# Kernel optimization log

Measured on AMD Instinct MI355X. Metric: run time of the kernel, lower is better.

The kernel has to match this reference:

```python
import jax, jax.numpy as jnp
import numpy as np

H = 4096          # hidden_size
I = 11008         # intermediate_size
G = 128           # AWQ group_size
# AWQ interleaved nibble order within each packed int32
_ORDER = jnp.array([0, 4, 1, 5, 2, 6, 3, 7], dtype=jnp.int32) * 4


def _mk_lin(key, K, N):
    k1, k2, k3 = jax.random.split(key, 3)
    qw = jax.random.randint(k1, (K, N // 8), 0, 100, dtype=jnp.int32)
    qz = jax.random.randint(k2, (K // G, N // 8), 0, 100, dtype=jnp.int32)
    sc = jax.random.normal(k3, (K // G, N), dtype=jnp.float32) * 0.02
    return qw, qz, sc


def setup_inputs() -> dict:
    key = jax.random.key(0)
    ks = jax.random.split(key, 7)
    x = jax.random.normal(ks[0], (8, 16, H), dtype=jnp.float32)
    ln1_w = jnp.ones((H,), dtype=jnp.float32)
    ln2_w = jnp.ones((H,), dtype=jnp.float32)
    qkv_qw, qkv_qz, qkv_sc = _mk_lin(ks[1], H, 3 * H)
    o_qw, o_qz, o_sc = _mk_lin(ks[2], H, H)
    gu_qw, gu_qz, gu_sc = _mk_lin(ks[3], H, 2 * I)
    dn_qw, dn_qz, dn_sc = _mk_lin(ks[4], I, H)
    return dict(x=x, ln1_w=ln1_w, ln2_w=ln2_w,
                qkv_qw=qkv_qw, qkv_qz=qkv_qz, qkv_sc=qkv_sc,
                o_qw=o_qw, o_qz=o_qz, o_sc=o_sc,
                gu_qw=gu_qw, gu_qz=gu_qz, gu_sc=gu_sc,
                dn_qw=dn_qw, dn_qz=dn_qz, dn_sc=dn_sc)


def rmsnorm(x, w, eps=1e-6):
    return x * jax.lax.rsqrt(jnp.mean(x * x, axis=-1, keepdims=True) + eps) * w


def dequant(qw, qz, sc):
    # qw: [K, N//8] int32 -> [K, N]; qz: [K//G, N//8] -> [K//G, N]
    K = qw.shape[0]
    N = sc.shape[1]
    w = ((qw[:, :, None] >> _ORDER) & 0xF).reshape(K, N).astype(sc.dtype)
    z = ((qz[:, :, None] >> _ORDER) & 0xF).reshape(K // G, N).astype(sc.dtype)
    return (w - jnp.repeat(z, G, axis=0)) * jnp.repeat(sc, G, axis=0)


def lite_linear(x, qw, qz, sc):
    return x @ dequant(qw, qz, sc)


def reference(x, ln1_w, ln2_w,
              qkv_qw, qkv_qz, qkv_sc,
              o_qw, o_qz, o_sc,
              gu_qw, gu_qz, gu_sc,
              dn_qw, dn_qz, dn_sc):
    residual = x
    h = rmsnorm(x, ln1_w)
    h = lite_linear(h, qkv_qw, qkv_qz, qkv_sc)[..., :H]  # mock attn: take q slice
    h = lite_linear(h, o_qw, o_qz, o_sc)
    h = residual + h
    residual = h
    h = rmsnorm(h, ln2_w)
    gate_up = lite_linear(h, gu_qw, gu_qz, gu_sc)
    gate, up = gate_up[..., :I], gate_up[..., I:]
    h = lite_linear(jax.nn.silu(gate) * up, dn_qw, dn_qz, dn_sc)
    return residual + h
```

## Files before the change

### kernel.cpp

```cpp
#include <hip/hip_runtime.h>

typedef unsigned int   u32;
typedef unsigned short u16;

typedef _Float16 h2  __attribute__((ext_vector_type(2)));
typedef _Float16 h8  __attribute__((ext_vector_type(8)));
typedef float    f32x4 __attribute__((ext_vector_type(4)));

#define M_TOK 128

__device__ __forceinline__ u16 f2h_(float f) {
    _Float16 h = (_Float16)f; return __builtin_bit_cast(u16, h);
}
__device__ __forceinline__ float h2f_(u16 b) {
    _Float16 h = __builtin_bit_cast(_Float16, b); return (float)h;
}
__device__ __forceinline__ void acc8(uint4 v, float* s) {
#pragma unroll
    for (int i = 0; i < 4; ++i) {
        u32 w = ((const u32*)&v)[i];
        s[2 * i]     += h2f_((u16)(w & 0xFFFF));
        s[2 * i + 1] += h2f_((u16)(w >> 16));
    }
}

__constant__ int SHC[8] = {0, 16, 4, 20, 8, 24, 12, 28};

__launch_bounds__(256)
__global__ void pack_zs(const int* __restrict__ qz, const float* __restrict__ sc,
                        u32* __restrict__ zs, int qws, int scs, int Ncols, int total) {
    const int idx = blockIdx.x * 256 + threadIdx.x;
    if (idx >= total) return;
    const int g = idx / Ncols, n = idx - g * Ncols;
    const u32 d = (u32)qz[(size_t)g * qws + (n >> 3)];
    const u32 zj = (d >> SHC[n & 7]) & 15u;
    const u32 mz = 0xE400u | zj;
    const u16 sh = f2h_(sc[(size_t)g * scs + n]);
    zs[(size_t)g * Ncols + n] = mz | ((u32)sh << 16);
}


__launch_bounds__(256)
__global__ void rmsnorm_k(const float* __restrict__ in, const float* __restrict__ w,
                          u16* __restrict__ out) {
    const int row = blockIdx.x;
    const float* x = in + (size_t)row * 4096;
    float ss = 0.f;
#pragma unroll
    for (int j = 0; j < 16; ++j) {
        float v = x[threadIdx.x + 256 * j];
        ss += v * v;
    }
#pragma unroll
    for (int off = 32; off > 0; off >>= 1) ss += __shfl_down(ss, off, 64);
    __shared__ float ws4[4];
    if ((threadIdx.x & 63) == 0) ws4[threadIdx.x >> 6] = ss;
    __syncthreads();
    float total = ws4[0] + ws4[1] + ws4[2] + ws4[3];
    float r = rsqrtf(total * (1.f / 4096.f) + 1e-6f);
    const int mt = row >> 4, l16 = row & 15;
#pragma unroll
    for (int c2 = 0; c2 < 2; ++c2) {
        int c = threadIdx.x * 2 + c2;
        int kb = c >> 2, qq = c & 3;
        u16 o8[8];
#pragma unroll
        for (int j = 0; j < 8; ++j) {
            int i = c * 8 + j;
            o8[j] = f2h_(x[i] * r * w[i]);
        }
        *(uint4*)(out + ((size_t)(kb * 8 + mt) * 64 + qq * 16 + l16) * 8) = *(const uint4*)o8;
    }
}

__launch_bounds__(256, 4)
__global__ void gemm_awq(const u16* __restrict__ A, const u32* __restrict__ zs,
                         const int* __restrict__ qw, u16* __restrict__ part,
                         int qws, int N, int K, int kchunk) {
    __shared__ __align__(16) char ldsB[4 * 4608];

    const int tid = threadIdx.x, w = tid >> 6, lane = tid & 63;
    const int q = lane >> 4, l16 = lane & 15;
    const int mh = w >> 1;
    const int bx = (blockIdx.x & 7) * (gridDim.x >> 3) + (blockIdx.x >> 3);
    const int n0w = bx * 64 + (w & 1) * 32;
    const int pc0 = n0w >> 3;
    const int kp = lane & 31, h = lane >> 5;
    const int sk = blockIdx.y, kc0 = sk * kchunk, kend = min(kc0 + kchunk, K);

    char* myB   = ldsB + w * 4608;
    char* wbase = myB + kp * 4;
    const u16* Ala = A + lane * 8;
    const int* qws_base = qw + pc0;
    const u32* zsA = zs + n0w + h * 8;
    const u32* zsB = zs + n0w + 16 + h * 8;

    f32x4 acc[4][2] = {};
    uint4 za0, za1, zb0, zb1;

    auto ldraw = [&](int k0) -> uint4 {
        return *(const uint4*)(qws_base + (size_t)(k0 + lane) * qws);
    };
    auto loadzs = [&](int g) {
        za0 = *(const uint4*)(zsA + (size_t)g * N);
        za1 = *(const uint4*)(zsA + (size_t)g * N + 4);
        zb0 = *(const uint4*)(zsB + (size_t)g * N);
        zb1 = *(const uint4*)(zsB + (size_t)g * N + 4);
    };
    auto route = [&](uint4 rv, u32* d) {
        const int i0 = kp * 8, i1 = i0 + 4;
        int b00 = __builtin_amdgcn_ds_bpermute(i0, (int)rv.x);
        int b10 = __builtin_amdgcn_ds_bpermute(i0, (int)rv.y);
        int b20 = __builtin_amdgcn_ds_bpermute(i0, (int)rv.z);
        int b30 = __builtin_amdgcn_ds_bpermute(i0, (int)rv.w);
        int b01 = __builtin_amdgcn_ds_bpermute(i1, (int)rv.x);
        int b11 = __builtin_amdgcn_ds_bpermute(i1, (int)rv.y);
        int b21 = __builtin_amdgcn_ds_bpermute(i1, (int)rv.z);
        int b31 = __builtin_amdgcn_ds_bpermute(i1, (int)rv.w);
        d[0] = (u32)(h ? b10 : b00);
        d[1] = (u32)(h ? b11 : b01);
        d[2] = (u32)(h ? b30 : b20);
        d[3] = (u32)(h ? b31 : b21);
    };
    auto emit8 = [&](u32 w0, u32 w1, int nb, uint4 z0, uint4 z1) {
        char* bb = wbase + nb * 144;
        u32 w0s = w0 >> 4, w1s = w1 >> 4;
        auto em = [&](int j, u32 a0, u32 a1, int b, u32 zsj) {
            h2 mz = __builtin_bit_cast(h2, __builtin_amdgcn_perm(zsj, zsj, 0x01000100u));
            h2 s2 = __builtin_bit_cast(h2, __builtin_amdgcn_perm(zsj, zsj, 0x03020302u));
            u32 t = __builtin_amdgcn_perm(a1, a0, (u32)(b | ((b + 4) << 16)));
            u32 u = (t & 0x000F000Fu) | 0x64006400u;
            h2 v = (__builtin_bit_cast(h2, u) + mz) * s2;
            *(u32*)(bb + j * 144) = __builtin_bit_cast(u32, v);
        };
        em(0, w0, w1, 0, z0.x);  em(4, w0, w1, 1, z1.x);
        em(1, w0, w1, 2, z0.y);  em(5, w0, w1, 3, z1.y);
        em(2, w0s, w1s, 0, z0.z); em(6, w0s, w1s, 1, z1.z);
        em(3, w0s, w1s, 2, z0.w); em(7, w0s, w1s, 3, z1.w);
    };
    auto dq = [&](uint4 rv) {
        u32 qd[4];
        route(rv, qd);
        emit8(qd[0], qd[1], h * 8, za0, za1);
        emit8(qd[2], qd[3], 16 + h * 8, zb0, zb1);
    };
    auto lda = [&](int k, uint4(&dst)[2][4]) {
        const int kb = k >> 5;
#pragma unroll
        for (int c = 0; c < 2; ++c)
#pragma unroll
            for (int mt = 0; mt < 4; ++mt)
                dst[c][mt] = *(const uint4*)(Ala + (size_t)((kb + c) * 8 + mh * 4 + mt) * 512);
    };

    uint4 rv_n = {0, 0, 0, 0};

    loadzs(kc0 >> 7);
    uint4 rv0 = ldraw(kc0);
    if (kc0 + 64 < kend) rv_n = ldraw(kc0 + 64);
    {
        u32 qd[4];
        route(rv0, qd);
        emit8(qd[0], qd[1], h * 8, za0, za1);
        emit8(qd[2], qd[3], 16 + h * 8, zb0, zb1);
    }
    if (((kc0 + 64) & 127) == 0 && kc0 + 64 < kend)
        loadzs((kc0 + 64) >> 7);

    for (int k0 = kc0; k0 < kend; k0 += 64) {
        __syncthreads();
        const bool kn1 = (k0 + 64) < kend, kn2 = (k0 + 128) < kend;
        uint4 af[2][4];
        lda(k0, af);
        uint4 bv[2][2];
#pragma unroll
        for (int c = 0; c < 2; ++c)
#pragma unroll
            for (int nt = 0; nt < 2; ++nt)
                bv[c][nt] = *(const uint4*)(myB + (nt * 16 + l16) * 144 + c * 64 + q * 16);
        uint4 rv_f = {0, 0, 0, 0};
        if (kn2) rv_f = ldraw(k0 + 128);
        if (kn1) {
            u32 qd[4];
            route(rv_n, qd);
            emit8(qd[0], qd[1], h * 8, za0, za1);
            emit8(qd[2], qd[3], 16 + h * 8, zb0, zb1);
        }
        if (kn2 && (((k0 + 128) & 127) == 0))
            loadzs((k0 + 128) >> 7);
#pragma unroll
        for (int c = 0; c < 2; ++c)
#pragma unroll
            for (int mt = 0; mt < 4; ++mt)
#pragma unroll
                for (int nt = 0; nt < 2; ++nt)
                    acc[mt][nt] = __builtin_amdgcn_mfma_f32_16x16x32_f16(
                        __builtin_bit_cast(h8, af[c][mt]),
                        __builtin_bit_cast(h8, bv[c][nt]),
                        acc[mt][nt], 0, 0, 0);
        rv_n = rv_f;
    }

    u16* pp = part + (size_t)sk * M_TOK * N;
#pragma unroll
    for (int mt = 0; mt < 4; ++mt)
#pragma unroll
        for (int nt = 0; nt < 2; ++nt) {
            const int n = n0w + nt * 16 + l16;
#pragma unroll
            for (int r = 0; r < 4; ++r) {
                const int m = (mh * 4 + mt) * 16 + q * 4 + r;
                pp[(size_t)m * N + n] = f2h_(acc[mt][nt][r]);
            }
        }
}

__launch_bounds__(256)
__global__ void reduce_to_afrag(const u16* __restrict__ part, u16* __restrict__ out,
                                int SK) {
    const int idx = blockIdx.x * 256 + threadIdx.x;
    const int m = idx >> 9, c = idx & 511;
    float s[8] = {};
    for (int k = 0; k < SK; ++k)
        acc8(*(const uint4*)(part + (size_t)k * 524288 + (size_t)m * 4096 + c * 8), s);
    const int kb = c >> 2, qq = c & 3, mt = m >> 4, l16 = m & 15;
    u16 o8[8];
#pragma unroll
    for (int j = 0; j < 8; ++j) o8[j] = f2h_(s[j]);
    *(uint4*)(out + ((size_t)(kb * 8 + mt) * 64 + qq * 16 + l16) * 8) = *(const uint4*)o8;
}

__launch_bounds__(256)
__global__ void reduce_add_f32(const u16* __restrict__ part, const float* __restrict__ resin,
                               float* __restrict__ out, int SK) {
    const int idx = blockIdx.x * 256 + threadIdx.x;
    const size_t base = (size_t)idx * 8;
    float s[8];
    *(float4*)&s[0] = *(const float4*)(resin + base);
    *(float4*)&s[4] = *(const float4*)(resin + base + 4);
    for (int k = 0; k < SK; ++k)
        acc8(*(const uint4*)(part + (size_t)k * 524288 + base), s);
    *(float4*)(out + base)     = *(const float4*)&s[0];
    *(float4*)(out + base + 4) = *(const float4*)&s[4];
}

__launch_bounds__(256)
__global__ void silu_mul(const u16* __restrict__ part, u16* __restrict__ act, int SK) {
    const int idx = blockIdx.x * 256 + threadIdx.x;
    const int m = idx / 1376, c = idx - m * 1376;
    const int nb = c * 8;
    float g[8] = {}, u[8] = {};
    for (int k = 0; k < SK; ++k) {
        const size_t base = (size_t)k * 2818048 + (size_t)m * 22016 + nb;
        acc8(*(const uint4*)(part + base), g);
        acc8(*(const uint4*)(part + base + 11008), u);
    }
    const int kb = nb >> 5, qq = (nb >> 3) & 3, mt = m >> 4, l16 = m & 15;
    u16 o8[8];
#pragma unroll
    for (int j = 0; j < 8; ++j) {
        float a = g[j] / (1.f + __expf(-g[j])) * u[j];
        o8[j] = f2h_(a);
    }
    *(uint4*)(act + ((size_t)(kb * 8 + mt) * 64 + qq * 16 + l16) * 8) = *(const uint4*)o8;
}

extern "C" void kernel_launch(void* const* d_in, const int* in_sizes, int n_in,
                              void* d_out, int out_size, void* d_ws, size_t ws_size,
                              hipStream_t stream) {
    const float* x      = (const float*)d_in[0];
    const float* ln1_w  = (const float*)d_in[1];
    const float* ln2_w  = (const float*)d_in[2];
    const int*   qkv_qw = (const int*)d_in[3];
    const int*   qkv_qz = (const int*)d_in[4];
    const float* qkv_sc = (const float*)d_in[5];
    const int*   o_qw   = (const int*)d_in[6];
    const int*   o_qz   = (const int*)d_in[7];
    const float* o_sc   = (const float*)d_in[8];
    const int*   gu_qw  = (const int*)d_in[9];
    const int*   gu_qz  = (const int*)d_in[10];
    const float* gu_sc  = (const float*)d_in[11];
    const int*   dn_qw  = (const int*)d_in[12];
    const int*   dn_qz  = (const int*)d_in[13];
    const float* dn_sc  = (const float*)d_in[14];
    float* out = (float*)d_out;

    char* ws = (char*)d_ws;
    u16*   pbuf = (u16*)(ws);
    u32*   zsb  = (u32*)(ws + 22544384);
    u16*   act  = (u16*)(ws + 25362432);
    float* res2 = (float*)(ws + 28180480);
    u16*   slot = (u16*)(ws + 30277632);

    rmsnorm_k<<<128, 256, 0, stream>>>(x, ln1_w, slot);
    pack_zs<<<512, 256, 0, stream>>>(qkv_qz, qkv_sc, zsb, 1536, 12288, 4096, 131072);

    gemm_awq<<<dim3(64, 16), 256, 0, stream>>>(slot, zsb, qkv_qw, pbuf,
                                               1536, 4096, 4096, 256);
    reduce_to_afrag<<<256, 256, 0, stream>>>(pbuf, slot, 16);
    pack_zs<<<512, 256, 0, stream>>>(o_qz, o_sc, zsb, 512, 4096, 4096, 131072);

    gemm_awq<<<dim3(64, 16), 256, 0, stream>>>(slot, zsb, o_qw, pbuf,
                                               512, 4096, 4096, 256);
    reduce_add_f32<<<256, 256, 0, stream>>>(pbuf, x, res2, 16);

    rmsnorm_k<<<128, 256, 0, stream>>>(res2, ln2_w, slot);
    pack_zs<<<2752, 256, 0, stream>>>(gu_qz, gu_sc, zsb, 2752, 22016, 22016, 704512);

    gemm_awq<<<dim3(344, 4), 256, 0, stream>>>(slot, zsb, gu_qw, pbuf,
                                               2752, 22016, 4096, 1024);
    silu_mul<<<688, 256, 0, stream>>>(pbuf, act, 4);
    pack_zs<<<1376, 256, 0, stream>>>(dn_qz, dn_sc, zsb, 512, 4096, 4096, 352256);

    gemm_awq<<<dim3(64, 20), 256, 0, stream>>>(act, zsb, dn_qw, pbuf,
                                               512, 4096, 11008, 576);
    reduce_add_f32<<<256, 256, 0, stream>>>(pbuf, res2, out, 20);
}
```

Before: 307.2 us.

## Share dequantized B tile across wave pairs with double-buffered LDS

Each pair of waves that covers the same 32 N-columns used to dequantize the whole B tile redundantly into private LDS. Now each wave dequantizes only half (16 columns, selected by mh) into a shared buffer, which halves the global qweight loads, bpermutes and dequant ALU per wave. To keep a single barrier per iteration, the LDS is split into two ping-pong buffers per N-half. This adds cross-wave dependence on the __syncthreads ordering for correctness.

```diff
diff --git a/kernel.cpp b/kernel.cpp
--- a/kernel.cpp
+++ b/kernel.cpp
@@ -81,49 +81,39 @@
 
     const int tid = threadIdx.x, w = tid >> 6, lane = tid & 63;
     const int q = lane >> 4, l16 = lane & 15;
-    const int mh = w >> 1;
+    const int mh = w >> 1, nh = w & 1;
     const int bx = (blockIdx.x & 7) * (gridDim.x >> 3) + (blockIdx.x >> 3);
-    const int n0w = bx * 64 + (w & 1) * 32;
+    const int n0w = bx * 64 + nh * 32;
     const int pc0 = n0w >> 3;
     const int kp = lane & 31, h = lane >> 5;
     const int sk = blockIdx.y, kc0 = sk * kchunk, kend = min(kc0 + kchunk, K);
 
-    char* myB   = ldsB + w * 4608;
-    char* wbase = myB + kp * 4;
+    char* buf0 = ldsB + nh * 9216;
+    char* buf1 = buf0 + 4608;
     const u16* Ala = A + lane * 8;
-    const int* qws_base = qw + pc0;
-    const u32* zsA = zs + n0w + h * 8;
-    const u32* zsB = zs + n0w + 16 + h * 8;
+    const int* qwp = qw + pc0 + mh * 2;
+    const u32* zsP = zs + n0w + mh * 16 + h * 8;
+    const int nbase = mh * 16 + h * 8;
 
     f32x4 acc[4][2] = {};
-    uint4 za0, za1, zb0, zb1;
-
-    auto ldraw = [&](int k0) -> uint4 {
-        return *(const uint4*)(qws_base + (size_t)(k0 + lane) * qws);
+    uint4 z0, z1;
+
+    auto ldraw = [&](int k0) -> uint2 {
+        return *(const uint2*)(qwp + (size_t)(k0 + lane) * qws);
     };
     auto loadzs = [&](int g) {
-        za0 = *(const uint4*)(zsA + (size_t)g * N);
-        za1 = *(const uint4*)(zsA + (size_t)g * N + 4);
-        zb0 = *(const uint4*)(zsB + (size_t)g * N);
-        zb1 = *(const uint4*)(zsB + (size_t)g * N + 4);
-    };
-    auto route = [&](uint4 rv, u32* d) {
+        z0 = *(const uint4*)(zsP + (size_t)g * N);
+        z1 = *(const uint4*)(zsP + (size_t)g * N + 4);
+    };
+    auto dq = [&](uint2 rv, char* buf) {
         const int i0 = kp * 8, i1 = i0 + 4;
         int b00 = __builtin_amdgcn_ds_bpermute(i0, (int)rv.x);
         int b10 = __builtin_amdgcn_ds_bpermute(i0, (int)rv.y);
-        int b20 = __builtin_amdgcn_ds_bpermute(i0, (int)rv.z);
-        int b30 = __builtin_amdgcn_ds_bpermute(i0, (int)rv.w);
         int b01 = __builtin_amdgcn_ds_bpermute(i1, (int)rv.x);
         int b11 = __builtin_amdgcn_ds_bpermute(i1, (int)rv.y);
-        int b21 = __builtin_amdgcn_ds_bpermute(i1, (int)rv.z);
-        int b31 = __builtin_amdgcn_ds_bpermute(i1, (int)rv.w);
-        d[0] = (u32)(h ? b10 : b00);
-        d[1] = (u32)(h ? b11 : b01);
-        d[2] = (u32)(h ? b30 : b20);
-        d[3] = (u32)(h ? b31 : b21);
-    };
-    auto emit8 = [&](u32 w0, u32 w1, int nb, uint4 z0, uint4 z1) {
-        char* bb = wbase + nb * 144;
+        u32 w0 = (u32)(h ? b10 : b00);
+        u32 w1 = (u32)(h ? b11 : b01);
+        char* bb = buf + kp * 4 + nbase * 144;
         u32 w0s = w0 >> 4, w1s = w1 >> 4;
         auto em = [&](int j, u32 a0, u32 a1, int b, u32 zsj) {
             h2 mz = __builtin_bit_cast(h2, __builtin_amdgcn_perm(zsj, zsj, 0x01000100u));
@@ -138,12 +128,6 @@
         em(2, w0s, w1s, 0, z0.z); em(6, w0s, w1s, 1, z1.z);
         em(3, w0s, w1s, 2, z0.w); em(7, w0s, w1s, 3, z1.w);
     };
-    auto dq = [&](uint4 rv) {
-        u32 qd[4];
-        route(rv, qd);
-        emit8(qd[0], qd[1], h * 8, za0, za1);
-        emit8(qd[2], qd[3], 16 + h * 8, zb0, zb1);
-    };
     auto lda = [&](int k, uint4(&dst)[2][4]) {
         const int kb = k >> 5;
 #pragma unroll
@@ -153,20 +137,16 @@
                 dst[c][mt] = *(const uint4*)(Ala + (size_t)((kb + c) * 8 + mh * 4 + mt) * 512);
     };
 
-    uint4 rv_n = {0, 0, 0, 0};
+    uint2 rv_n = {0, 0};
 
     loadzs(kc0 >> 7);
-    uint4 rv0 = ldraw(kc0);
+    uint2 rv0 = ldraw(kc0);
     if (kc0 + 64 < kend) rv_n = ldraw(kc0 + 64);
-    {
-        u32 qd[4];
-        route(rv0, qd);
-        emit8(qd[0], qd[1], h * 8, za0, za1);
-        emit8(qd[2], qd[3], 16 + h * 8, zb0, zb1);
-    }
+    dq(rv0, buf0);
     if (((kc0 + 64) & 127) == 0 && kc0 + 64 < kend)
         loadzs((kc0 + 64) >> 7);
 
+    char* cur = buf0; char* nxt = buf1;
     for (int k0 = kc0; k0 < kend; k0 += 64) {
         __syncthreads();
         const bool kn1 = (k0 + 64) < kend, kn2 = (k0 + 128) < kend;
@@ -177,15 +157,10 @@
         for (int c = 0; c < 2; ++c)
 #pragma unroll
             for (int nt = 0; nt < 2; ++nt)
-                bv[c][nt] = *(const uint4*)(myB + (nt * 16 + l16) * 144 + c * 64 + q * 16);
-        uint4 rv_f = {0, 0, 0, 0};
+                bv[c][nt] = *(const uint4*)(cur + (nt * 16 + l16) * 144 + c * 64 + q * 16);
+        uint2 rv_f = {0, 0};
         if (kn2) rv_f = ldraw(k0 + 128);
-        if (kn1) {
-            u32 qd[4];
-            route(rv_n, qd);
-            emit8(qd[0], qd[1], h * 8, za0, za1);
-            emit8(qd[2], qd[3], 16 + h * 8, zb0, zb1);
-        }
+        if (kn1) dq(rv_n, nxt);
         if (kn2 && (((k0 + 128) & 127) == 0))
             loadzs((k0 + 128) >> 7);
 #pragma unroll
@@ -199,6 +174,7 @@
                         __builtin_bit_cast(h8, bv[c][nt]),
                         acc[mt][nt], 0, 0, 0);
         rv_n = rv_f;
+        char* t = cur; cur = nxt; nxt = t;
     }
 
     u16* pp = part + (size_t)sk * M_TOK * N;
```

New measurement: 299.9 us. 1.02x faster.

## Give each wave all 128 rows with double-buffered private LDS, dropping block barriers

Applied to the files above, without the earlier changes.

Each wave now computes all 8 M-tiles (128 tokens) for its own 32-column strip, so a block covers 128 columns and the grids are halved. Every dequantized weight tile is therefore used by all tokens without duplicating dequant work across waves. Each wave's LDS slice is double-buffered, which lets the per-iteration __syncthreads be removed: a wave writes the next tile while reading the current one. The XCD block remap is generalized for grid sizes not divisible by 8. The cost is doubled accumulator registers, more A-fragment loads per wave, occupancy lowered to 3 blocks, and fewer blocks in flight.

```diff
diff --git a/kernel.cpp b/kernel.cpp
--- a/kernel.cpp
+++ b/kernel.cpp
@@ -73,29 +73,30 @@
     }
 }
 
-__launch_bounds__(256, 4)
+__launch_bounds__(256, 3)
 __global__ void gemm_awq(const u16* __restrict__ A, const u32* __restrict__ zs,
                          const int* __restrict__ qw, u16* __restrict__ part,
                          int qws, int N, int K, int kchunk) {
-    __shared__ __align__(16) char ldsB[4 * 4608];
+    __shared__ __align__(16) char ldsB[4 * 9216];
 
     const int tid = threadIdx.x, w = tid >> 6, lane = tid & 63;
     const int q = lane >> 4, l16 = lane & 15;
-    const int mh = w >> 1;
-    const int bx = (blockIdx.x & 7) * (gridDim.x >> 3) + (blockIdx.x >> 3);
-    const int n0w = bx * 64 + (w & 1) * 32;
+    const int nwg = gridDim.x, bid = blockIdx.x;
+    const int qq8 = nwg >> 3, r8 = nwg & 7, xcd = bid & 7, boff = bid >> 3;
+    const int bx = (xcd < r8 ? xcd * (qq8 + 1) : r8 * (qq8 + 1) + (xcd - r8) * qq8) + boff;
+    const int n0w = bx * 128 + w * 32;
     const int pc0 = n0w >> 3;
     const int kp = lane & 31, h = lane >> 5;
     const int sk = blockIdx.y, kc0 = sk * kchunk, kend = min(kc0 + kchunk, K);
 
-    char* myB   = ldsB + w * 4608;
-    char* wbase = myB + kp * 4;
+    char* buf0 = ldsB + w * 9216;
+    char* buf1 = buf0 + 4608;
     const u16* Ala = A + lane * 8;
     const int* qws_base = qw + pc0;
     const u32* zsA = zs + n0w + h * 8;
     const u32* zsB = zs + n0w + 16 + h * 8;
 
-    f32x4 acc[4][2] = {};
+    f32x4 acc[8][2] = {};
     uint4 za0, za1, zb0, zb1;
 
     auto ldraw = [&](int k0) -> uint4 {
@@ -107,7 +108,7 @@
         zb0 = *(const uint4*)(zsB + (size_t)g * N);
         zb1 = *(const uint4*)(zsB + (size_t)g * N + 4);
     };
-    auto route = [&](uint4 rv, u32* d) {
+    auto dq = [&](uint4 rv, char* buf) {
         const int i0 = kp * 8, i1 = i0 + 4;
         int b00 = __builtin_amdgcn_ds_bpermute(i0, (int)rv.x);
         int b10 = __builtin_amdgcn_ds_bpermute(i0, (int)rv.y);
@@ -117,40 +118,28 @@
         int b11 = __builtin_amdgcn_ds_bpermute(i1, (int)rv.y);
         int b21 = __builtin_amdgcn_ds_bpermute(i1, (int)rv.z);
         int b31 = __builtin_amdgcn_ds_bpermute(i1, (int)rv.w);
-        d[0] = (u32)(h ? b10 : b00);
-        d[1] = (u32)(h ? b11 : b01);
-        d[2] = (u32)(h ? b30 : b20);
-        d[3] = (u32)(h ? b31 : b21);
-    };
-    auto emit8 = [&](u32 w0, u32 w1, int nb, uint4 z0, uint4 z1) {
-        char* bb = wbase + nb * 144;
-        u32 w0s = w0 >> 4, w1s = w1 >> 4;
-        auto em = [&](int j, u32 a0, u32 a1, int b, u32 zsj) {
-            h2 mz = __builtin_bit_cast(h2, __builtin_amdgcn_perm(zsj, zsj, 0x01000100u));
-            h2 s2 = __builtin_bit_cast(h2, __builtin_amdgcn_perm(zsj, zsj, 0x03020302u));
-            u32 t = __builtin_amdgcn_perm(a1, a0, (u32)(b | ((b + 4) << 16)));
-            u32 u = (t & 0x000F000Fu) | 0x64006400u;
-            h2 v = (__builtin_bit_cast(h2, u) + mz) * s2;
-            *(u32*)(bb + j * 144) = __builtin_bit_cast(u32, v);
+        u32 qd0 = (u32)(h ? b10 : b00);
+        u32 qd1 = (u32)(h ? b11 : b01);
+        u32 qd2 = (u32)(h ? b30 : b20);
+        u32 qd3 = (u32)(h ? b31 : b21);
+        auto emit8 = [&](u32 w0, u32 w1, int nb, uint4 z0, uint4 z1) {
+            char* bb = buf + kp * 4 + nb * 144;
+            u32 w0s = w0 >> 4, w1s = w1 >> 4;
+            auto em = [&](int j, u32 a0, u32 a1, int b, u32 zsj) {
+                h2 mz = __builtin_bit_cast(h2, __builtin_amdgcn_perm(zsj, zsj, 0x01000100u));
+                h2 s2 = __builtin_bit_cast(h2, __builtin_amdgcn_perm(zsj, zsj, 0x03020302u));
+                u32 t = __builtin_amdgcn_perm(a1, a0, (u32)(b | ((b + 4) << 16)));
+                u32 u = (t & 0x000F000Fu) | 0x64006400u;
+                h2 v = (__builtin_bit_cast(h2, u) + mz) * s2;
+                *(u32*)(bb + j * 144) = __builtin_bit_cast(u32, v);
+            };
+            em(0, w0, w1, 0, z0.x);  em(4, w0, w1, 1, z1.x);
+            em(1, w0, w1, 2, z0.y);  em(5, w0, w1, 3, z1.y);
+            em(2, w0s, w1s, 0, z0.z); em(6, w0s, w1s, 1, z1.z);
+            em(3, w0s, w1s, 2, z0.w); em(7, w0s, w1s, 3, z1.w);
         };
-        em(0, w0, w1, 0, z0.x);  em(4, w0, w1, 1, z1.x);
-        em(1, w0, w1, 2, z0.y);  em(5, w0, w1, 3, z1.y);
-        em(2, w0s, w1s, 0, z0.z); em(6, w0s, w1s, 1, z1.z);
-        em(3, w0s, w1s, 2, z0.w); em(7, w0s, w1s, 3, z1.w);
-    };
-    auto dq = [&](uint4 rv) {
-        u32 qd[4];
-        route(rv, qd);
-        emit8(qd[0], qd[1], h * 8, za0, za1);
-        emit8(qd[2], qd[3], 16 + h * 8, zb0, zb1);
-    };
-    auto lda = [&](int k, uint4(&dst)[2][4]) {
-        const int kb = k >> 5;
-#pragma unroll
-        for (int c = 0; c < 2; ++c)
-#pragma unroll
-            for (int mt = 0; mt < 4; ++mt)
-                dst[c][mt] = *(const uint4*)(Ala + (size_t)((kb + c) * 8 + mh * 4 + mt) * 512);
+        emit8(qd0, qd1, h * 8, za0, za1);
+        emit8(qd2, qd3, 16 + h * 8, zb0, zb1);
     };
 
     uint4 rv_n = {0, 0, 0, 0};
@@ -158,58 +147,51 @@
     loadzs(kc0 >> 7);
     uint4 rv0 = ldraw(kc0);
     if (kc0 + 64 < kend) rv_n = ldraw(kc0 + 64);
-    {
-        u32 qd[4];
-        route(rv0, qd);
-        emit8(qd[0], qd[1], h * 8, za0, za1);
-        emit8(qd[2], qd[3], 16 + h * 8, zb0, zb1);
-    }
+    dq(rv0, buf0);
     if (((kc0 + 64) & 127) == 0 && kc0 + 64 < kend)
         loadzs((kc0 + 64) >> 7);
 
+    char* cur = buf0; char* nxt = buf1;
     for (int k0 = kc0; k0 < kend; k0 += 64) {
-        __syncthreads();
         const bool kn1 = (k0 + 64) < kend, kn2 = (k0 + 128) < kend;
-        uint4 af[2][4];
-        lda(k0, af);
-        uint4 bv[2][2];
-#pragma unroll
-        for (int c = 0; c < 2; ++c)
-#pragma unroll
-            for (int nt = 0; nt < 2; ++nt)
-                bv[c][nt] = *(const uint4*)(myB + (nt * 16 + l16) * 144 + c * 64 + q * 16);
         uint4 rv_f = {0, 0, 0, 0};
         if (kn2) rv_f = ldraw(k0 + 128);
-        if (kn1) {
-            u32 qd[4];
-            route(rv_n, qd);
-            emit8(qd[0], qd[1], h * 8, za0, za1);
-            emit8(qd[2], qd[3], 16 + h * 8, zb0, zb1);
-        }
+        if (kn1) dq(rv_n, nxt);
         if (kn2 && (((k0 + 128) & 127) == 0))
             loadzs((k0 + 128) >> 7);
-#pragma unroll
-        for (int c = 0; c < 2; ++c)
-#pragma unroll
-            for (int mt = 0; mt < 4; ++mt)
+        const int kb = k0 >> 5;
+#pragma unroll
+        for (int c = 0; c < 2; ++c) {
+            uint4 bvc[2];
+#pragma unroll
+            for (int nt = 0; nt < 2; ++nt)
+                bvc[nt] = *(const uint4*)(cur + (nt * 16 + l16) * 144 + c * 64 + q * 16);
+            uint4 afc[8];
+#pragma unroll
+            for (int mt = 0; mt < 8; ++mt)
+                afc[mt] = *(const uint4*)(Ala + (size_t)((kb + c) * 8 + mt) * 512);
+#pragma unroll
+            for (int mt = 0; mt < 8; ++mt)
 #pragma unroll
                 for (int nt = 0; nt < 2; ++nt)
                     acc[mt][nt] = __builtin_amdgcn_mfma_f32_16x16x32_f16(
-                        __builtin_bit_cast(h8, af[c][mt]),
-                        __builtin_bit_cast(h8, bv[c][nt]),
+                        __builtin_bit_cast(h8, afc[mt]),
+                        __builtin_bit_cast(h8, bvc[nt]),
                         acc[mt][nt], 0, 0, 0);
+        }
         rv_n = rv_f;
+        char* t = cur; cur = nxt; nxt = t;
     }
 
     u16* pp = part + (size_t)sk * M_TOK * N;
 #pragma unroll
-    for (int mt = 0; mt < 4; ++mt)
+    for (int mt = 0; mt < 8; ++mt)
 #pragma unroll
         for (int nt = 0; nt < 2; ++nt) {
             const int n = n0w + nt * 16 + l16;
 #pragma unroll
             for (int r = 0; r < 4; ++r) {
-                const int m = (mh * 4 + mt) * 16 + q * 4 + r;
+                const int m = mt * 16 + q * 4 + r;
                 pp[(size_t)m * N + n] = f2h_(acc[mt][nt][r]);
             }
         }
@@ -295,24 +277,24 @@
     rmsnorm_k<<<128, 256, 0, stream>>>(x, ln1_w, slot);
     pack_zs<<<512, 256, 0, stream>>>(qkv_qz, qkv_sc, zsb, 1536, 12288, 4096, 131072);
 
-    gemm_awq<<<dim3(64, 16), 256, 0, stream>>>(slot, zsb, qkv_qw, pbuf,
+    gemm_awq<<<dim3(32, 16), 256, 0, stream>>>(slot, zsb, qkv_qw, pbuf,
                                                1536, 4096, 4096, 256);
     reduce_to_afrag<<<256, 256, 0, stream>>>(pbuf, slot, 16);
     pack_zs<<<512, 256, 0, stream>>>(o_qz, o_sc, zsb, 512, 4096, 4096, 131072);
 
-    gemm_awq<<<dim3(64, 16), 256, 0, stream>>>(slot, zsb, o_qw, pbuf,
+    gemm_awq<<<dim3(32, 16), 256, 0, stream>>>(slot, zsb, o_qw, pbuf,
                                                512, 4096, 4096, 256);
     reduce_add_f32<<<256, 256, 0, stream>>>(pbuf, x, res2, 16);
 
     rmsnorm_k<<<128, 256, 0, stream>>>(res2, ln2_w, slot);
     pack_zs<<<2752, 256, 0, stream>>>(gu_qz, gu_sc, zsb, 2752, 22016, 22016, 704512);
 
-    gemm_awq<<<dim3(344, 4), 256, 0, stream>>>(slot, zsb, gu_qw, pbuf,
+    gemm_awq<<<dim3(172, 4), 256, 0, stream>>>(slot, zsb, gu_qw, pbuf,
                                                2752, 22016, 4096, 1024);
     silu_mul<<<688, 256, 0, stream>>>(pbuf, act, 4);
     pack_zs<<<1376, 256, 0, stream>>>(dn_qz, dn_sc, zsb, 512, 4096, 4096, 352256);
 
-    gemm_awq<<<dim3(64, 20), 256, 0, stream>>>(act, zsb, dn_qw, pbuf,
+    gemm_awq<<<dim3(32, 20), 256, 0, stream>>>(act, zsb, dn_qw, pbuf,
                                                512, 4096, 11008, 576);
     reduce_add_f32<<<256, 256, 0, stream>>>(pbuf, res2, out, 20);
 }
```

Result: no change. 311.2 us (+1.3%).
